# Optimization experiments

Hardware: AMD Instinct MI355X
Metric: run time of the kernel (lower is better)

## Reference

```python
import jax, jax.numpy as jnp
import numpy as np
from jax import lax

B, N, C = 32, 4096, 512
HEADS, K, U = 4, 16, 4
V = C // HEADS  # 128
KS = 7
EPS = 1e-3  # keras LayerNormalization default epsilon


def _layernorm(x, g, b):
    mu = jnp.mean(x, axis=-1, keepdims=True)
    var = jnp.var(x, axis=-1, keepdims=True)
    return (x - mu) * lax.rsqrt(var + EPS) * g + b


def setup_inputs() -> dict:
    key = jax.random.key(0)
    ks = jax.random.split(key, 6)
    sc = lambda fan: 1.0 / np.sqrt(fan)
    x = jax.random.normal(ks[0], (B, N, C), dtype=jnp.float32)
    wq = jax.random.normal(ks[1], (C, K * HEADS), dtype=jnp.float32) * sc(C)
    wk = jax.random.normal(ks[2], (C, K * U), dtype=jnp.float32) * sc(C)
    wv = jax.random.normal(ks[3], (C, V * U), dtype=jnp.float32) * sc(C)
    gq = jnp.ones((K * HEADS,), jnp.float32)
    bq = jnp.zeros((K * HEADS,), jnp.float32)
    gv = jnp.ones((V * U,), jnp.float32)
    bv = jnp.zeros((V * U,), jnp.float32)
    pos_w = jax.random.normal(ks[4], (1, KS, U, K), dtype=jnp.float32) * sc(KS * U)
    pos_b = jnp.zeros((K,), jnp.float32)
    return {"x": x, "wq": wq, "wk": wk, "wv": wv, "gq": gq, "bq": bq,
            "gv": gv, "bv": bv, "pos_w": pos_w, "pos_b": pos_b}


def reference(x, wq, wk, wv, gq, bq, gv, bv, pos_w, pos_b):
    # 1x1 conv projections == per-position matmuls
    q = _layernorm(x @ wq, gq, bq)                      # (B, N, K*HEADS)
    k = x @ wk                                          # (B, N, K*U)
    v = _layernorm(x @ wv, gv, bv)                      # (B, N, V*U)
    # rearranges (Reshape + Permute((2,3,1)))
    q = q.reshape(B, N, HEADS, K).transpose(0, 2, 3, 1)  # (B, H, K, N)
    k = k.reshape(B, N, U, K).transpose(0, 2, 3, 1)      # (B, U, K, N)
    v = v.reshape(B, N, U, V).transpose(0, 2, 3, 1)      # (B, U, V, N)
    k = jax.nn.softmax(k, axis=-1)                       # softmax over positions n
    # content lambda
    lc = jnp.einsum('bukn,buvn->bkv', k, v)              # (B, K, V)
    yc = jnp.einsum('bhkn,bkv->bnhv', q, lc)             # (B, N, H, V)
    # positional lambda: Conv2D(K, (1, KS), 'same') over (B, V, N, U) NHWC
    v2 = v.transpose(0, 2, 3, 1)                         # (B, V, N, U)
    lp = lax.conv_general_dilated(v2, pos_w, (1, 1), 'SAME',
                                  dimension_numbers=('NHWC', 'HWIO', 'NHWC')) + pos_b  # (B, V, N, K)
    lp = lp.transpose(0, 1, 3, 2)                        # (B, V, K, N)
    yp = jnp.einsum('bhkn,bvkn->bnhv', q, lp)            # (B, N, H, V)
    return (yc + yp).reshape(B, N, HEADS * V)            # (B, N, out_dim)
```

## Files before the change

### kernel.cpp

```cpp
#include <hip/hip_runtime.h>
#include <hip/hip_bf16.h>


#define Bb   32
#define Nn   4096
#define Cc   512
#define Hh   4
#define Kk   16
#define Uu   4
#define Vv   128
#define QKVW 640
#define EPSf 1e-3f

typedef __bf16 bf16;
typedef bf16  bf16x8 __attribute__((ext_vector_type(8)));
typedef bf16  bf16x4 __attribute__((ext_vector_type(4)));
typedef float f32x4  __attribute__((ext_vector_type(4)));

#define WT_OFF   0UL
#define QKV_OFF  655360UL
#define QMU_OFF  168427520UL
#define QRS_OFF  168951808UL
#define VMU_OFF  169476096UL
#define VRS_OFF  170000384UL
#define KPM_OFF  170524672UL
#define KPS_OFF  170590208UL
#define KMX_OFF  170655744UL
#define KIV_OFF  170663936UL
#define LCP_OFF  170672128UL
#define LC_OFF   174866432UL

__device__ inline float bf2f(bf16 x) { return (float)x; }

__global__ __launch_bounds__(256) void k0_weights(
    const float* __restrict__ wq, const float* __restrict__ wk,
    const float* __restrict__ wv, bf16* __restrict__ wt)
{
    int idx = blockIdx.x * 256 + threadIdx.x;
    if (idx >= Cc * QKVW) return;
    int c = idx / QKVW, j = idx % QKVW;
    float v;
    if (j < 64)       v = wq[c * 64 + j];
    else if (j < 128) v = wk[c * 64 + (j - 64)];
    else              v = wv[c * 512 + (j - 128)];
    wt[(size_t)j * Cc + c] = (bf16)v;
}

__global__ __launch_bounds__(256) void k1_gemm(
    const float* __restrict__ x, const bf16* __restrict__ wt,
    bf16* __restrict__ qkv)
{
    int bid = blockIdx.x;
    int swz = (bid & 7) * 640 + (bid >> 3);
    int bm = swz / 5, bn = swz % 5;
    int row0 = bm * 128, col0 = bn * 128;

    int tid  = threadIdx.x;
    int lane = tid & 63, w = tid >> 6;
    int wr = (w >> 1) * 64, wc = (w & 1) * 64;
    int l15 = lane & 15, g = lane >> 4;

    __shared__ __align__(16) bf16 As[128 * 64];
    __shared__ __align__(16) bf16 Bs[128 * 64];

    f32x4 acc[4][4];
#pragma unroll
    for (int m = 0; m < 4; ++m)
#pragma unroll
        for (int c = 0; c < 4; ++c) { acc[m][c][0]=0.f; acc[m][c][1]=0.f; acc[m][c][2]=0.f; acc[m][c][3]=0.f; }

    const int ar  = tid >> 3;
    const int as  = tid & 7;
    const int asw = ((as ^ (ar & 7)) * 8);
    const float* aptr = x + (size_t)(row0 + ar) * Cc + as * 8;

    const int brl = lane >> 3;
    const int bsl = lane & 7;

    f32x4 pA[4][2];
#pragma unroll
    for (int it = 0; it < 4; ++it) {
        const float* src = aptr + (size_t)it * 32 * Cc;
        pA[it][0] = *(const f32x4*)src;
        pA[it][1] = *(const f32x4*)(src + 4);
    }

    for (int kt = 0; kt < 8; ++kt) {
        const int kb = kt * 64;
        __syncthreads();
#pragma unroll
        for (int it = 0; it < 4; ++it) {
            int r = it * 32 + ar;
            bf16x8 pk;
            pk[0]=(bf16)pA[it][0][0]; pk[1]=(bf16)pA[it][0][1];
            pk[2]=(bf16)pA[it][0][2]; pk[3]=(bf16)pA[it][0][3];
            pk[4]=(bf16)pA[it][1][0]; pk[5]=(bf16)pA[it][1][1];
            pk[6]=(bf16)pA[it][1][2]; pk[7]=(bf16)pA[it][1][3];
            *(bf16x8*)&As[r * 64 + asw] = pk;
        }
#pragma unroll
        for (int i = 0; i < 4; ++i) {
            int grp = w * 4 + i;
            int row = grp * 8 + brl;
            const bf16* src = wt + (size_t)(col0 + row) * Cc + kb + ((bsl ^ (row & 7)) * 8);
            __builtin_amdgcn_global_load_lds((const void*)src,
                                             (void*)((char*)Bs + grp * 1024), 16, 0, 0);
        }
        if (kt < 7) {
#pragma unroll
            for (int it = 0; it < 4; ++it) {
                const float* src = aptr + (size_t)it * 32 * Cc + (kb + 64);
                pA[it][0] = *(const f32x4*)src;
                pA[it][1] = *(const f32x4*)(src + 4);
            }
        }
        __syncthreads();
#pragma unroll
        for (int kk = 0; kk < 2; ++kk) {
            bf16x8 aF[4], bF[4];
#pragma unroll
            for (int m = 0; m < 4; ++m) {
                int r = wr + 16 * m + l15;
                aF[m] = *(const bf16x8*)&As[r * 64 + (((kk * 4 + g) ^ (r & 7)) * 8)];
            }
#pragma unroll
            for (int c = 0; c < 4; ++c) {
                int r = wc + 16 * c + l15;
                bF[c] = *(const bf16x8*)&Bs[r * 64 + (((kk * 4 + g) ^ (r & 7)) * 8)];
            }
#pragma unroll
            for (int m = 0; m < 4; ++m)
#pragma unroll
                for (int c = 0; c < 4; ++c)
                    acc[m][c] = __builtin_amdgcn_mfma_f32_16x16x32_bf16(aF[m], bF[c], acc[m][c], 0, 0, 0);
        }
    }
#pragma unroll
    for (int m = 0; m < 4; ++m)
#pragma unroll
        for (int c = 0; c < 4; ++c) {
            int grow = row0 + wr + 16 * m + (lane >> 4) * 4;
            int gcol = col0 + wc + 16 * c + l15;
#pragma unroll
            for (int r = 0; r < 4; ++r)
                qkv[(size_t)(grow + r) * QKVW + gcol] = (bf16)acc[m][c][r];
        }
}

__global__ __launch_bounds__(256) void k2a_kpart(
    const bf16* __restrict__ qkv, float* __restrict__ kpm, float* __restrict__ kps)
{
    int ns = blockIdx.x;
    int b  = blockIdx.y;
    int t  = threadIdx.x;
    int c0 = (t & 7) * 8;
    int stripe = t >> 3;
    float m[8], s[8];
#pragma unroll
    for (int j = 0; j < 8; ++j) { m[j] = -1e30f; s[j] = 0.f; }
    for (int i = 0; i < 16; ++i) {
        int n = ns * 512 + stripe + i * 32;
        bf16x8 kv = *(const bf16x8*)(qkv + (size_t)(b * Nn + n) * QKVW + 64 + c0);
#pragma unroll
        for (int j = 0; j < 8; ++j) {
            float f = bf2f(kv[j]);
            float mn = fmaxf(m[j], f);
            s[j] = s[j] * __expf(m[j] - mn) + __expf(f - mn);
            m[j] = mn;
        }
    }
    __shared__ float pm[64 * 32], ps[64 * 32];
#pragma unroll
    for (int j = 0; j < 8; ++j) { pm[(c0 + j) * 32 + stripe] = m[j]; ps[(c0 + j) * 32 + stripe] = s[j]; }
    __syncthreads();
    if (t < 64) {
        float M = -1e30f;
        for (int i = 0; i < 32; ++i) M = fmaxf(M, pm[t * 32 + i]);
        float S = 0.f;
        for (int i = 0; i < 32; ++i) S += ps[t * 32 + i] * __expf(pm[t * 32 + i] - M);
        kpm[(b * 8 + ns) * 64 + t] = M;
        kps[(b * 8 + ns) * 64 + t] = S;
    }
}

__global__ __launch_bounds__(256) void k2a2_kfinal(
    const float* __restrict__ kpm, const float* __restrict__ kps,
    float* __restrict__ kmax, float* __restrict__ kinv)
{
    int idx = blockIdx.x * 256 + threadIdx.x;
    if (idx >= 2048) return;
    int b = idx >> 6, c = idx & 63;
    float M = -1e30f;
#pragma unroll
    for (int ns = 0; ns < 8; ++ns) M = fmaxf(M, kpm[(b * 8 + ns) * 64 + c]);
    float S = 0.f;
#pragma unroll
    for (int ns = 0; ns < 8; ++ns) S += kps[(b * 8 + ns) * 64 + c] * __expf(kpm[(b * 8 + ns) * 64 + c] - M);
    kmax[idx] = M;
    kinv[idx] = 1.0f / S;
}

__global__ __launch_bounds__(256) void k2b_lnstats(
    const bf16* __restrict__ qkv, float* __restrict__ qmu, float* __restrict__ qrs,
    float* __restrict__ vmu, float* __restrict__ vrs)
{
    int row = blockIdx.x * 256 + threadIdx.x;
    const bf16* p = qkv + (size_t)row * QKVW;
    float s = 0.f, ss = 0.f;
#pragma unroll
    for (int i = 0; i < 8; ++i) {
        bf16x8 v = *(const bf16x8*)(p + i * 8);
#pragma unroll
        for (int j = 0; j < 8; ++j) { float f = bf2f(v[j]); s += f; ss += f * f; }
    }
    float mu = s * (1.f / 64.f);
    float var = ss * (1.f / 64.f) - mu * mu;
    qmu[row] = mu; qrs[row] = rsqrtf(var + EPSf);
    s = 0.f; ss = 0.f;
#pragma unroll
    for (int i = 0; i < 64; ++i) {
        bf16x8 v = *(const bf16x8*)(p + 128 + i * 8);
#pragma unroll
        for (int j = 0; j < 8; ++j) { float f = bf2f(v[j]); s += f; ss += f * f; }
    }
    mu = s * (1.f / 512.f);
    var = ss * (1.f / 512.f) - mu * mu;
    vmu[row] = mu; vrs[row] = rsqrtf(var + EPSf);
}

__global__ __launch_bounds__(256) void k3_lc(
    const bf16* __restrict__ qkv, const float* __restrict__ kmax, const float* __restrict__ kinv,
    const float* __restrict__ vmu, const float* __restrict__ vrs,
    const float* __restrict__ gv, const float* __restrict__ bv,
    float* __restrict__ lcp)
{
    int ns = blockIdx.x;
    int b  = blockIdx.y;
    int t  = threadIdx.x;

    __shared__ __align__(16) float vln[16 * 512];
    __shared__ float smk[16 * 64];
    __shared__ float gvl[512], bvl[512];
    for (int i = t; i < 512; i += 256) { gvl[i] = gv[i]; bvl[i] = bv[i]; }

    int kk = t >> 4, vg = t & 15;
    float acc[8];
#pragma unroll
    for (int j = 0; j < 8; ++j) acc[j] = 0.f;

    for (int ch = 0; ch < 16; ++ch) {
        int nb = ns * 256 + ch * 16;
        __syncthreads();
        {
            int c0  = (t & 63) * 8;
            int nl0 = t >> 6;
#pragma unroll
            for (int i = 0; i < 4; ++i) {
                int nl = nl0 + i * 4;
                int row = b * Nn + nb + nl;
                bf16x8 v8 = *(const bf16x8*)(qkv + (size_t)row * QKVW + 128 + c0);
                float mu = vmu[row], rs = vrs[row];
#pragma unroll
                for (int j = 0; j < 8; ++j)
                    vln[nl * 512 + c0 + j] = (bf2f(v8[j]) - mu) * rs * gvl[c0 + j] + bvl[c0 + j];
            }
        }
        {
            int c0 = (t & 15) * 4;
            int nl = t >> 4;
            int row = b * Nn + nb + nl;
            bf16x4 k4 = *(const bf16x4*)(qkv + (size_t)row * QKVW + 64 + c0);
#pragma unroll
            for (int j = 0; j < 4; ++j)
                smk[nl * 64 + c0 + j] = __expf(bf2f(k4[j]) - kmax[b * 64 + c0 + j]) * kinv[b * 64 + c0 + j];
        }
        __syncthreads();
#pragma unroll 4
        for (int nl = 0; nl < 16; ++nl) {
#pragma unroll
            for (int u = 0; u < 4; ++u) {
                float sm = smk[nl * 64 + u * 16 + kk];
                f32x4 a = *(const f32x4*)&vln[nl * 512 + u * 128 + vg * 8];
                f32x4 c = *(const f32x4*)&vln[nl * 512 + u * 128 + vg * 8 + 4];
                acc[0] += sm * a[0]; acc[1] += sm * a[1]; acc[2] += sm * a[2]; acc[3] += sm * a[3];
                acc[4] += sm * c[0]; acc[5] += sm * c[1]; acc[6] += sm * c[2]; acc[7] += sm * c[3];
            }
        }
    }
    float* dst = lcp + (size_t)(b * 16 + ns) * 2048 + kk * 128 + vg * 8;
#pragma unroll
    for (int j = 0; j < 8; ++j) dst[j] = acc[j];
}

__global__ __launch_bounds__(256) void k3b_lcreduce(
    const float* __restrict__ lcp, float* __restrict__ lc)
{
    int idx = blockIdx.x * 256 + threadIdx.x;
    int b = idx >> 11, cc = idx & 2047;
    float s = 0.f;
#pragma unroll
    for (int ns = 0; ns < 16; ++ns) s += lcp[(size_t)(b * 16 + ns) * 2048 + cc];
    lc[idx] = s;
}

#define TN4    16
#define NPAN4  15
#define PELEM  1056

__global__ __launch_bounds__(256) void k4_out(
    const bf16* __restrict__ qkv, const float* __restrict__ qmu, const float* __restrict__ qrs,
    const float* __restrict__ vmu, const float* __restrict__ vrs,
    const float* __restrict__ gq, const float* __restrict__ bq,
    const float* __restrict__ gv, const float* __restrict__ bv,
    const float* __restrict__ posw, const float* __restrict__ posb,
    const float* __restrict__ lc, float* __restrict__ out)
{
    const int nt = blockIdx.x, b = blockIdx.y, t = threadIdx.x;
    const int n0 = nt * TN4;

    __shared__ __align__(16) bf16 PN[NPAN4 * PELEM];
    __shared__ __align__(16) bf16 Ax[64 * 104];
    __shared__ __align__(16) bf16 PP[4 * 256];

    bf16x8 z8;
#pragma unroll
    for (int j = 0; j < 8; ++j) z8[j] = (bf16)0.f;
    for (int i = t; i < 832; i += 256) *(bf16x8*)&Ax[i * 8] = z8;
    if (t < 128) *(bf16x8*)&PP[t * 8] = z8;
    __syncthreads();

    if (t < 64) {
        int g = t >> 5, du = t & 31;
        if (du < 28) {
            f32x4 a = *(const f32x4*)(posw + du * 16 + g * 8);
            f32x4 c = *(const f32x4*)(posw + du * 16 + g * 8 + 4);
            bf16x8 pk;
            pk[0]=(bf16)a[0]; pk[1]=(bf16)a[1]; pk[2]=(bf16)a[2]; pk[3]=(bf16)a[3];
            pk[4]=(bf16)c[0]; pk[5]=(bf16)c[1]; pk[6]=(bf16)c[2]; pk[7]=(bf16)c[3];
            *(bf16x8*)&PP[g * 256 + du * 8] = pk;
        }
    }
    {
        int p = t >> 7, v = t & 127;
        const float* src = lc + b * 2048 + p * 8 * 128 + v;
        bf16x8 pk;
#pragma unroll
        for (int j = 0; j < 8; ++j) pk[j] = (bf16)src[j * 128];
        *(bf16x8*)&PN[p * PELEM + v * 8] = pk;
        if (t < 128) {
            bf16x8 ones = z8; ones[0] = (bf16)1.0f;
            *(bf16x8*)&PN[2 * PELEM + t * 8] = ones;
            *(bf16x8*)&PN[3 * PELEM + t * 8] = z8;
        }
    }
    for (int it = t; it < 22 * 16; it += 256) {
        int lr = it >> 4, vo = it & 15;
        int n  = n0 - 3 + lr;
        int pbase = (4 + (lr >> 1)) * PELEM + (lr & 1) * 4;
        if ((unsigned)n < (unsigned)Nn) {
            int row = b * Nn + n;
            float mu = vmu[row], rs = vrs[row];
            float f[4][8];
#pragma unroll
            for (int u = 0; u < 4; ++u) {
                bf16x8 v8 = *(const bf16x8*)(qkv + (size_t)row * QKVW + 128 + u * 128 + vo * 8);
                f32x4 g0 = *(const f32x4*)(gv + u * 128 + vo * 8);
                f32x4 g1 = *(const f32x4*)(gv + u * 128 + vo * 8 + 4);
                f32x4 b0 = *(const f32x4*)(bv + u * 128 + vo * 8);
                f32x4 b1 = *(const f32x4*)(bv + u * 128 + vo * 8 + 4);
#pragma unroll
                for (int j = 0; j < 4; ++j) f[u][j]     = (bf2f(v8[j])     - mu) * rs * g0[j] + b0[j];
#pragma unroll
                for (int j = 0; j < 4; ++j) f[u][4 + j] = (bf2f(v8[4 + j]) - mu) * rs * g1[j] + b1[j];
            }
#pragma unroll
            for (int vi = 0; vi < 8; ++vi) {
                bf16x4 pk;
                pk[0]=(bf16)f[0][vi]; pk[1]=(bf16)f[1][vi]; pk[2]=(bf16)f[2][vi]; pk[3]=(bf16)f[3][vi];
                *(bf16x4*)&PN[pbase + (vo * 8 + vi) * 8] = pk;
            }
        } else {
            bf16x4 zz; zz[0]=(bf16)0.f; zz[1]=(bf16)0.f; zz[2]=(bf16)0.f; zz[3]=(bf16)0.f;
#pragma unroll
            for (int vi = 0; vi < 8; ++vi)
                *(bf16x4*)&PN[pbase + (vo * 8 + vi) * 8] = zz;
        }
    }
    if (t < 128) {
        int row = t >> 1, half = t & 1;
        int n = n0 + (row >> 2), h = row & 3;
        int gr = b * Nn + n;
        int c0 = h * 16 + half * 8;
        bf16x8 q8 = *(const bf16x8*)(qkv + (size_t)gr * QKVW + c0);
        float mu = qmu[gr], rs = qrs[gr];
        f32x4 gg0 = *(const f32x4*)(gq + c0), gg1 = *(const f32x4*)(gq + c0 + 4);
        f32x4 bb0 = *(const f32x4*)(bq + c0), bb1 = *(const f32x4*)(bq + c0 + 4);
        f32x4 pb0 = *(const f32x4*)(posb + half * 8), pb1 = *(const f32x4*)(posb + half * 8 + 4);
        float qbp = 0.f;
        bf16x8 pk;
#pragma unroll
        for (int j = 0; j < 4; ++j) {
            float f = (bf2f(q8[j]) - mu) * rs * gg0[j] + bb0[j];
            qbp += f * pb0[j]; pk[j] = (bf16)f;
        }
#pragma unroll
        for (int j = 0; j < 4; ++j) {
            float f = (bf2f(q8[4 + j]) - mu) * rs * gg1[j] + bb1[j];
            qbp += f * pb1[j]; pk[4 + j] = (bf16)f;
        }
        *(bf16x8*)&Ax[row * 104 + half * 8] = pk;
        float qb = qbp + __shfl_xor(qbp, 1);
        if (!half) Ax[row * 104 + 16] = (bf16)qb;
    }
    __syncthreads();

    const int lane = t & 63, rt = t >> 6;
    const int g = lane >> 4, l15 = lane & 15;
    const int arow = rt * 16 + l15;

    bf16x8 aF0 = *(const bf16x8*)&Ax[arow * 104 + g * 8];
    f32x4 zf; zf[0]=0.f; zf[1]=0.f; zf[2]=0.f; zf[3]=0.f;
#pragma unroll
    for (int ct = 0; ct < 2; ++ct) {
        bf16x8 bp = *(const bf16x8*)&PP[g * 256 + (ct * 16 + l15) * 8];
        f32x4 rf = __builtin_amdgcn_mfma_f32_16x16x32_bf16(aF0, bp, zf, 0, 0, 0);
        int du = ct * 16 + l15;
#pragma unroll
        for (int reg = 0; reg < 4; ++reg) {
            int row = rt * 16 + g * 4 + reg;
            Ax[row * 104 + 32 + g * 4 + du] = (bf16)rf[reg];
        }
    }

    bf16x8 aF1 = *(const bf16x8*)&Ax[arow * 104 + 32 + g * 8];
    bf16x8 aF2 = *(const bf16x8*)&Ax[arow * 104 + 64 + g * 8];
    const int P1 = (4 + rt * 2 + g) * PELEM;
    const int P2 = (4 + rt * 2 + 4) * PELEM;
    f32x4 acc[8];
#pragma unroll
    for (int c = 0; c < 8; ++c) acc[c] = zf;
#pragma unroll
    for (int c = 0; c < 8; ++c) {
        int vb = (c * 16 + l15) * 8;
        bf16x8 b0 = *(const bf16x8*)&PN[g * PELEM + vb];
        bf16x8 b1 = *(const bf16x8*)&PN[P1 + vb];
        bf16x8 b2 = *(const bf16x8*)&PN[P2 + vb];
        acc[c] = __builtin_amdgcn_mfma_f32_16x16x32_bf16(aF0, b0, acc[c], 0, 0, 0);
        acc[c] = __builtin_amdgcn_mfma_f32_16x16x32_bf16(aF1, b1, acc[c], 0, 0, 0);
        acc[c] = __builtin_amdgcn_mfma_f32_16x16x32_bf16(aF2, b2, acc[c], 0, 0, 0);
    }
#pragma unroll
    for (int c = 0; c < 8; ++c) {
#pragma unroll
        for (int reg = 0; reg < 4; ++reg) {
            int row = rt * 16 + g * 4 + reg;
            int n = n0 + (row >> 2), h = row & 3;
            out[((size_t)(b * Nn + n)) * 512 + h * 128 + c * 16 + l15] = acc[c][reg];
        }
    }
}

extern "C" void kernel_launch(void* const* d_in, const int* in_sizes, int n_in,
                              void* d_out, int out_size, void* d_ws, size_t ws_size,
                              hipStream_t stream) {
    const float* x    = (const float*)d_in[0];
    const float* wq   = (const float*)d_in[1];
    const float* wk   = (const float*)d_in[2];
    const float* wv   = (const float*)d_in[3];
    const float* gq   = (const float*)d_in[4];
    const float* bq   = (const float*)d_in[5];
    const float* gv   = (const float*)d_in[6];
    const float* bv   = (const float*)d_in[7];
    const float* posw = (const float*)d_in[8];
    const float* posb = (const float*)d_in[9];
    float* out = (float*)d_out;

    char* ws = (char*)d_ws;
    bf16*  wt   = (bf16*)(ws + WT_OFF);
    bf16*  qkv  = (bf16*)(ws + QKV_OFF);
    float* qmu  = (float*)(ws + QMU_OFF);
    float* qrs  = (float*)(ws + QRS_OFF);
    float* vmu  = (float*)(ws + VMU_OFF);
    float* vrs  = (float*)(ws + VRS_OFF);
    float* kpm  = (float*)(ws + KPM_OFF);
    float* kps  = (float*)(ws + KPS_OFF);
    float* kmax = (float*)(ws + KMX_OFF);
    float* kinv = (float*)(ws + KIV_OFF);
    float* lcp  = (float*)(ws + LCP_OFF);
    float* lc   = (float*)(ws + LC_OFF);

    k0_weights<<<(Cc * QKVW + 255) / 256, 256, 0, stream>>>(wq, wk, wv, wt);
    k1_gemm<<<5120, 256, 0, stream>>>(x, wt, qkv);
    k2a_kpart<<<dim3(8, 32), 256, 0, stream>>>(qkv, kpm, kps);
    k2a2_kfinal<<<8, 256, 0, stream>>>(kpm, kps, kmax, kinv);
    k2b_lnstats<<<512, 256, 0, stream>>>(qkv, qmu, qrs, vmu, vrs);
    k3_lc<<<dim3(16, 32), 256, 0, stream>>>(qkv, kmax, kinv, vmu, vrs, gv, bv, lcp);
    k3b_lcreduce<<<256, 256, 0, stream>>>(lcp, lc);
    k4_out<<<dim3(Nn / TN4, Bb), 256, 0, stream>>>(qkv, qmu, qrs, vmu, vrs, gq, bq, gv, bv,
                                                   posw, posb, lc, out);
}
```

Measured before the change: 460.7 us.

## Pre-convert x to bf16 and load GEMM tiles directly into LDS

Adds a separate pass that converts the fp32 input x to a bf16 copy in workspace. The projection GEMM can then stream A and B tiles straight into shared memory with global_load_lds instead of loading fp32 and converting in registers. The goal is to cut register traffic and per-tile conversion work in the GEMM main loop, and halve the A-operand bytes it reads. In exchange it adds an extra full read of x plus a bf16 write, and it needs a larger workspace; it falls back to the old kernel if the workspace is too small.

```diff
diff --git a/kernel.cpp b/kernel.cpp
--- a/kernel.cpp
+++ b/kernel.cpp
@@ -29,6 +29,8 @@
 #define KIV_OFF  170663936UL
 #define LCP_OFF  170672128UL
 #define LC_OFF   174866432UL
+#define XB_OFF   175128576UL
+#define WS_NEED  309346304UL
 
 __device__ inline float bf2f(bf16 x) { return (float)x; }
 
@@ -46,7 +48,103 @@
     wt[(size_t)j * Cc + c] = (bf16)v;
 }
 
-__global__ __launch_bounds__(256) void k1_gemm(
+__global__ __launch_bounds__(256) void k0x_cvt(
+    const float* __restrict__ x, bf16* __restrict__ xb)
+{
+    const size_t total = (size_t)Bb * Nn * Cc / 8;
+    for (size_t i = (size_t)blockIdx.x * 256 + threadIdx.x; i < total;
+         i += (size_t)gridDim.x * 256) {
+        const float* s = x + i * 8;
+        f32x4 a = *(const f32x4*)s;
+        f32x4 b = *(const f32x4*)(s + 4);
+        bf16x8 pk;
+        pk[0]=(bf16)a[0]; pk[1]=(bf16)a[1]; pk[2]=(bf16)a[2]; pk[3]=(bf16)a[3];
+        pk[4]=(bf16)b[0]; pk[5]=(bf16)b[1]; pk[6]=(bf16)b[2]; pk[7]=(bf16)b[3];
+        *(bf16x8*)(xb + i * 8) = pk;
+    }
+}
+
+__global__ __launch_bounds__(256) void k1_gemm_fast(
+    const bf16* __restrict__ xb, const bf16* __restrict__ wt,
+    bf16* __restrict__ qkv)
+{
+    int bid = blockIdx.x;
+    int swz = (bid & 7) * 640 + (bid >> 3);
+    int bm = swz / 5, bn = swz % 5;
+    int row0 = bm * 128, col0 = bn * 128;
+
+    int tid  = threadIdx.x;
+    int lane = tid & 63, w = tid >> 6;
+    int wr = (w >> 1) * 64, wc = (w & 1) * 64;
+    int l15 = lane & 15, g = lane >> 4;
+
+    __shared__ __align__(16) bf16 As[128 * 64];
+    __shared__ __align__(16) bf16 Bs[128 * 64];
+
+    f32x4 acc[4][4];
+#pragma unroll
+    for (int m = 0; m < 4; ++m)
+#pragma unroll
+        for (int c = 0; c < 4; ++c) { acc[m][c][0]=0.f; acc[m][c][1]=0.f; acc[m][c][2]=0.f; acc[m][c][3]=0.f; }
+
+    const int srow = lane >> 3;
+    const int ssl  = lane & 7;
+    const int sslw = (ssl ^ srow) * 8;
+
+    const bf16* aBase = xb + (size_t)(row0 + srow) * Cc + sslw;
+    const bf16* bBase = wt + (size_t)(col0 + srow) * Cc + sslw;
+
+    for (int kt = 0; kt < 8; ++kt) {
+        const int kb = kt * 64;
+        __syncthreads();
+#pragma unroll
+        for (int i = 0; i < 4; ++i) {
+            int grp = w * 4 + i;
+            __builtin_amdgcn_global_load_lds(
+                (const void*)(aBase + (size_t)grp * 8 * Cc + kb),
+                (void*)((char*)As + grp * 1024), 16, 0, 0);
+        }
+#pragma unroll
+        for (int i = 0; i < 4; ++i) {
+            int grp = w * 4 + i;
+            __builtin_amdgcn_global_load_lds(
+                (const void*)(bBase + (size_t)grp * 8 * Cc + kb),
+                (void*)((char*)Bs + grp * 1024), 16, 0, 0);
+        }
+        __syncthreads();
+#pragma unroll
+        for (int kk = 0; kk < 2; ++kk) {
+            bf16x8 aF[4], bF[4];
+#pragma unroll
+            for (int m = 0; m < 4; ++m) {
+                int r = wr + 16 * m + l15;
+                aF[m] = *(const bf16x8*)&As[r * 64 + (((kk * 4 + g) ^ (r & 7)) * 8)];
+            }
+#pragma unroll
+            for (int c = 0; c < 4; ++c) {
+                int r = wc + 16 * c + l15;
+                bF[c] = *(const bf16x8*)&Bs[r * 64 + (((kk * 4 + g) ^ (r & 7)) * 8)];
+            }
+#pragma unroll
+            for (int m = 0; m < 4; ++m)
+#pragma unroll
+                for (int c = 0; c < 4; ++c)
+                    acc[m][c] = __builtin_amdgcn_mfma_f32_16x16x32_bf16(aF[m], bF[c], acc[m][c], 0, 0, 0);
+        }
+    }
+#pragma unroll
+    for (int m = 0; m < 4; ++m)
+#pragma unroll
+        for (int c = 0; c < 4; ++c) {
+            int grow = row0 + wr + 16 * m + g * 4;
+            int gcol = col0 + wc + 16 * c + l15;
+#pragma unroll
+            for (int r = 0; r < 4; ++r)
+                qkv[(size_t)(grow + r) * QKVW + gcol] = (bf16)acc[m][c][r];
+        }
+}
+
+__global__ __launch_bounds__(256) void k1_gemm_legacy(
     const float* __restrict__ x, const bf16* __restrict__ wt,
     bf16* __restrict__ qkv)
 {
@@ -139,7 +237,7 @@
     for (int m = 0; m < 4; ++m)
 #pragma unroll
         for (int c = 0; c < 4; ++c) {
-            int grow = row0 + wr + 16 * m + (lane >> 4) * 4;
+            int grow = row0 + wr + 16 * m + g * 4;
             int gcol = col0 + wc + 16 * c + l15;
 #pragma unroll
             for (int r = 0; r < 4; ++r)
@@ -488,9 +586,15 @@
     float* kinv = (float*)(ws + KIV_OFF);
     float* lcp  = (float*)(ws + LCP_OFF);
     float* lc   = (float*)(ws + LC_OFF);
+    bf16*  xb   = (bf16*)(ws + XB_OFF);
 
     k0_weights<<<(Cc * QKVW + 255) / 256, 256, 0, stream>>>(wq, wk, wv, wt);
-    k1_gemm<<<5120, 256, 0, stream>>>(x, wt, qkv);
+    if (ws_size >= WS_NEED) {
+        k0x_cvt<<<4096, 256, 0, stream>>>(x, xb);
+        k1_gemm_fast<<<5120, 256, 0, stream>>>(xb, wt, qkv);
+    } else {
+        k1_gemm_legacy<<<5120, 256, 0, stream>>>(x, wt, qkv);
+    }
     k2a_kpart<<<dim3(8, 32), 256, 0, stream>>>(qkv, kpm, kps);
     k2a2_kfinal<<<8, 256, 0, stream>>>(kpm, kps, kmax, kinv);
     k2b_lnstats<<<512, 256, 0, stream>>>(qkv, qmu, qrs, vmu, vrs);
```

Measured after the change: 470.3 us. 2.1% more time.
